# Performance work log

Measured on AMD Instinct MI355X. Metric: run time of the kernel, lower is better.

## Reference

```python
import jax, jax.numpy as jnp
import numpy as np
from jax import lax

PIXEL_MAX = 255.0  # PSNR reference intensity, matches I=255 in the torch source


def setup_inputs() -> dict:
    key = jax.random.key(0)
    k1, k2 = jax.random.split(key)
    # RGBA image and RGBA kernel, 0..255 pixel range (PSNR uses I=255)
    x = jax.random.uniform(k1, (1, 4, 2048, 2048), dtype=jnp.float32) * PIXEL_MAX
    kernel = jax.random.uniform(k2, (1, 4, 16, 16), dtype=jnp.float32) * PIXEL_MAX
    return {"x": x, "kernel": kernel}


def reference(x, kernel):
    """Fused equivalent of: unfold every (Hk,Wk) window, alpha-blend it with the
    kernel using the kernel's alpha channel, then per-window PSNR vs the kernel.

    alpha_blend(x_win, k, a) = (1-a)*x_win + a*k  with a = k_alpha/255, so
    blended - k = (1-a)*(x_win - k), hence per-window per-channel MSE is a
    weighted sliding-window sum: mean_ij w_ij*(x-k)^2 with w = (1-a)^2.
    Expanding (x-k)^2 lets us use three depthwise VALID correlations instead of
    materializing the [L,C,Hk,Wk] unfold+repeat tensor.
    """
    C, Hk, Wk = kernel.shape[1], kernel.shape[2], kernel.shape[3]
    k = kernel[0]                       # (C, Hk, Wk)
    alpha = k[3] / PIXEL_MAX            # (Hk, Wk), alpha plane (channel 3)
    w = (1.0 - alpha) ** 2              # per-tap weight, shared across channels

    dn = ("NCHW", "OIHW", "NCHW")
    w_dw = jnp.broadcast_to(w, (C, 1, Hk, Wk))   # depthwise weights
    kw_dw = (k * w)[:, None]                      # (C, 1, Hk, Wk)

    def corr(inp, wt):
        return lax.conv_general_dilated(
            inp, wt, window_strides=(1, 1), padding="VALID",
            dimension_numbers=dn, feature_group_count=C)

    Sxx = corr(x * x, w_dw)                        # (1, C, H', W') sum w*x^2
    Sxk = corr(x, kw_dw)                           # (1, C, H', W') sum w*x*k
    Skk = jnp.sum(k * k * w, axis=(-2, -1))[None, :, None, None]  # sum w*k^2

    mse = (Sxx - 2.0 * Sxk + Skk) / (Hk * Wk)      # (1, C, H', W')
    psnr = jnp.mean(20.0 * jnp.log10(PIXEL_MAX / jnp.sqrt(mse)), axis=1)  # mean over C
    return psnr[0]                                  # (H-Hk+1, W-Wk+1)
```

## Files before the change

kernel.cpp:

```cpp
#include <hip/hip_runtime.h>
#include <hip/hip_bf16.h>
#include <math.h>

#define XDIM 2048
#define OW   2033
#define TR   32
#define TC   256
#define XWP  272
#define PH   16

typedef __bf16 bf16x8 __attribute__((ext_vector_type(8)));
typedef float  f32x16 __attribute__((ext_vector_type(16)));

union U128 { uint4 u; bf16x8 v; };

__device__ __forceinline__ unsigned short bfbits(float f) {
    return __builtin_bit_cast(unsigned short, __float2bfloat16(f));
}
__device__ __forceinline__ unsigned int packx(float f) {
    return ((unsigned int)bfbits(f) << 16) | (unsigned int)bfbits(f * f);
}
__device__ __forceinline__ int slz(int c) {
    return c ^ (((c >> 2) & 7) << 1);
}

__global__ __launch_bounds__(256) void psnr_mfma_kernel(
    const float* __restrict__ x,
    const float* __restrict__ kern,
    float* __restrict__ out)
{
    __shared__ __align__(16) uint2 xtp[PH][XWP];
    __shared__ __align__(16) unsigned int wt[4][17 * 20];
    __shared__ float skkArr[4];

    const int tid  = threadIdx.x;
    const int lane = tid & 63;
    const int wv   = tid >> 6;
    const int nn   = lane & 31;
    const int hf   = lane >> 5;

    const int r0 = blockIdx.y * TR;
    const int c0 = blockIdx.x * TC;

    {
        float k0 = kern[tid], k1 = kern[256 + tid], k2 = kern[512 + tid], k3 = kern[768 + tid];
        float a  = k3 * (1.0f / 255.0f);
        float om = 1.0f - a;
        float w  = om * om;
        int i = tid >> 4, j = tid & 15;
        unsigned int wlo = (unsigned int)bfbits(w);
        wt[0][i * 20 + j] = ((unsigned int)bfbits(-2.0f * w * k0) << 16) | wlo;
        wt[1][i * 20 + j] = ((unsigned int)bfbits(-2.0f * w * k1) << 16) | wlo;
        wt[2][i * 20 + j] = ((unsigned int)bfbits(-2.0f * w * k2) << 16) | wlo;
        wt[3][i * 20 + j] = ((unsigned int)bfbits(-2.0f * w * k3) << 16) | wlo;
        if (tid < 80) {
            int c = tid / 20, wd = tid % 20;
            wt[c][16 * 20 + wd] = 0u;
        }
        float4* red = reinterpret_cast<float4*>(&xtp[0][0]);
        red[tid] = make_float4(w*k0*k0, w*k1*k1, w*k2*k2, w*k3*k3);
        __syncthreads();
        #pragma unroll
        for (int s = 128; s > 0; s >>= 1) {
            if (tid < s) {
                float4 o = red[tid + s], m = red[tid];
                m.x += o.x; m.y += o.y; m.z += o.z; m.w += o.w;
                red[tid] = m;
            }
            __syncthreads();
        }
        if (tid == 0) {
            float4 r0v = red[0];
            skkArr[0] = r0v.x; skkArr[1] = r0v.y; skkArr[2] = r0v.z; skkArr[3] = r0v.w;
        }
    }

    f32x16 psum0, psum1;
    #pragma unroll
    for (int q = 0; q < 16; ++q) { psum0[q] = 0.0f; psum1[q] = 0.0f; }

    const int xbase = nn + 4 * hf;
    const int wvoff = (wv << 6);
    const int p0 = slz(xbase)      + wvoff, p1 = slz(xbase + 2)  + wvoff;
    const int p2 = slz(xbase + 8)  + wvoff, p3 = slz(xbase + 10) + wvoff;
    const int p4 = slz(xbase + 32) + wvoff, p5 = slz(xbase + 34) + wvoff;
    const int p6 = slz(xbase + 40) + wvoff, p7 = slz(xbase + 42) + wvoff;

    for (int ch = 0; ch < 4; ++ch) {
        const float* __restrict__ xc = x + ((size_t)ch << 22);

        f32x16 acc0, acc1;
        #pragma unroll
        for (int q = 0; q < 16; ++q) { acc0[q] = 0.0f; acc1[q] = 0.0f; }

        #pragma unroll
        for (int ph = 0; ph < 3; ++ph) {
            const int base = ph * PH;
            const int nr   = (ph == 2) ? 15 : 16;

            __syncthreads();
            for (int idx = tid; idx < nr * 68; idx += 256) {
                int row = idx / 68;
                int it  = idx - row * 68;
                int gr  = r0 + base + row; if (gr > XDIM - 1) gr = XDIM - 1;
                int gc  = c0 + it * 4;
                const float* rp = xc + (size_t)gr * XDIM;
                float4 v;
                if (gc + 3 <= XDIM - 1) {
                    v = *reinterpret_cast<const float4*>(rp + gc);
                } else {
                    int e0 = gc     < XDIM ? gc     : XDIM - 1;
                    int e1 = gc + 1 < XDIM ? gc + 1 : XDIM - 1;
                    int e2 = gc + 2 < XDIM ? gc + 2 : XDIM - 1;
                    int e3 = gc + 3 < XDIM ? gc + 3 : XDIM - 1;
                    v = make_float4(rp[e0], rp[e1], rp[e2], rp[e3]);
                }
                int e4 = gc + 4 < XDIM ? gc + 4 : XDIM - 1;
                float x4 = rp[e4];

                unsigned int P0 = packx(v.x), P1 = packx(v.y), P2 = packx(v.z),
                             P3 = packx(v.w), P4 = packx(x4);
                int s   = (it & 7) << 1;
                int sl0 = (4 * it)     ^ s;
                int sl2 = (4 * it + 2) ^ s;
                uint2* bb = &xtp[row][0];
                *reinterpret_cast<uint4*>(bb + sl0) = make_uint4(P0, P1, P1, P2);
                *reinterpret_cast<uint4*>(bb + sl2) = make_uint4(P2, P3, P3, P4);
            }
            __syncthreads();

            const unsigned int* __restrict__ wch = &wt[ch][0];
            for (int r = 0; r < nr; ++r) {
                int ip = base + r;
                unsigned int d = (unsigned int)(ip - nn);
                unsigned int wrow = (d > 15u) ? 16u : d;
                U128 alo, ahi;
                alo.u = *reinterpret_cast<const uint4*>(wch + wrow * 20 + hf * 4);
                ahi.u = *reinterpret_cast<const uint4*>(wch + wrow * 20 + 8 + hf * 4);

                const uint2* __restrict__ bp = &xtp[r][0];
                U128 blo0, bhi0, blo1, bhi1;
                { uint2 a0 = bp[p0], a1 = bp[p1]; blo0.u = make_uint4(a0.x, a0.y, a1.x, a1.y); }
                { uint2 a0 = bp[p2], a1 = bp[p3]; bhi0.u = make_uint4(a0.x, a0.y, a1.x, a1.y); }
                { uint2 a0 = bp[p4], a1 = bp[p5]; blo1.u = make_uint4(a0.x, a0.y, a1.x, a1.y); }
                { uint2 a0 = bp[p6], a1 = bp[p7]; bhi1.u = make_uint4(a0.x, a0.y, a1.x, a1.y); }

                acc0 = __builtin_amdgcn_mfma_f32_32x32x16_bf16(alo.v, blo0.v, acc0, 0, 0, 0);
                acc0 = __builtin_amdgcn_mfma_f32_32x32x16_bf16(ahi.v, bhi0.v, acc0, 0, 0, 0);
                acc1 = __builtin_amdgcn_mfma_f32_32x32x16_bf16(alo.v, blo1.v, acc1, 0, 0, 0);
                acc1 = __builtin_amdgcn_mfma_f32_32x32x16_bf16(ahi.v, bhi1.v, acc1, 0, 0, 0);
            }
        }

        float sk = skkArr[ch];
        #pragma unroll
        for (int q = 0; q < 16; ++q) {
            float m0 = (acc0[q] + sk) * (1.0f / 256.0f);
            float m1 = (acc1[q] + sk) * (1.0f / 256.0f);
            psum0[q] += __log2f(m0);
            psum1[q] += __log2f(m1);
        }
    }

    const float BASE = 48.130803608679344f;
    const float SC   = 2.5f * 0.3010299956639812f;
    const int col0 = c0 + (wv << 6) + nn;
    const int col1 = col0 + 32;
    #pragma unroll
    for (int q = 0; q < 16; ++q) {
        int row = r0 + (q & 3) + ((q >> 2) << 3) + (hf << 2);
        if (row < OW) {
            float* orow = out + (size_t)row * OW;
            if (col0 < OW) orow[col0] = BASE - SC * psum0[q];
            if (col1 < OW) orow[col1] = BASE - SC * psum1[q];
        }
    }
}

extern "C" void kernel_launch(void* const* d_in, const int* in_sizes, int n_in,
                              void* d_out, int out_size, void* d_ws, size_t ws_size,
                              hipStream_t stream) {
    (void)in_sizes; (void)n_in; (void)d_ws; (void)ws_size; (void)out_size;
    const float* x    = (const float*)d_in[0];
    const float* kern = (const float*)d_in[1];
    float* out        = (float*)d_out;

    dim3 grid(XDIM / TC, (OW + TR - 1) / TR);
    psnr_mfma_kernel<<<grid, 256, 0, stream>>>(x, kern, out);
}
```

Measured before the change: 66.09 us.

## Double-buffer LDS tiles with register prefetch across flattened channel/phase loop

Flattens the channel and row-phase loops into one 12-step pipeline and double-buffers the packed bf16 tile in shared memory. Global loads for step p+2 are issued into registers while step p+1 is packed and written, which overlaps memory latency with MFMA work and halves the barriers per step. Packing now uses a single v_cvt_pk_bf16_f32 instruction. The cost is doubled LDS and more live registers, which may lower occupancy. The last phase now loads 16 rows instead of 15.

After: 68.08 us. +3.0%, slower.

```diff
diff --git a/kernel.cpp b/kernel.cpp
--- a/kernel.cpp
+++ b/kernel.cpp
@@ -8,6 +8,7 @@
 #define TC   256
 #define XWP  272
 #define PH   16
+#define NP   12
 
 typedef __bf16 bf16x8 __attribute__((ext_vector_type(8)));
 typedef float  f32x16 __attribute__((ext_vector_type(16)));
@@ -18,7 +19,9 @@
     return __builtin_bit_cast(unsigned short, __float2bfloat16(f));
 }
 __device__ __forceinline__ unsigned int packx(float f) {
-    return ((unsigned int)bfbits(f) << 16) | (unsigned int)bfbits(f * f);
+    unsigned int r;
+    asm("v_cvt_pk_bf16_f32 %0, %1, %2" : "=v"(r) : "v"(f * f), "v"(f));
+    return r;
 }
 __device__ __forceinline__ int slz(int c) {
     return c ^ (((c >> 2) & 7) << 1);
@@ -29,7 +32,7 @@
     const float* __restrict__ kern,
     float* __restrict__ out)
 {
-    __shared__ __align__(16) uint2 xtp[PH][XWP];
+    __shared__ __align__(16) uint2 xtp[2][PH][XWP];
     __shared__ __align__(16) unsigned int wt[4][17 * 20];
     __shared__ float skkArr[4];
 
@@ -41,6 +44,60 @@
 
     const int r0 = blockIdx.y * TR;
     const int c0 = blockIdx.x * TC;
+
+    float4 pf[5];
+    float  pe[5];
+
+    auto issue = [&](int p) {
+        int ch = p / 3, ph = p - 3 * ch;
+        const float* __restrict__ xc = x + ((size_t)ch << 22);
+        const int rbase = r0 + ph * PH;
+        #pragma unroll
+        for (int t = 0; t < 5; ++t) {
+            int idx = tid + 256 * t;
+            if (idx < PH * 68) {
+                int row = idx / 68;
+                int it  = idx - row * 68;
+                int gr  = rbase + row; if (gr > XDIM - 1) gr = XDIM - 1;
+                int gc  = c0 + it * 4;
+                const float* rp = xc + (size_t)gr * XDIM;
+                if (gc + 3 <= XDIM - 1) {
+                    pf[t] = *reinterpret_cast<const float4*>(rp + gc);
+                } else {
+                    int e0 = gc     < XDIM ? gc     : XDIM - 1;
+                    int e1 = gc + 1 < XDIM ? gc + 1 : XDIM - 1;
+                    int e2 = gc + 2 < XDIM ? gc + 2 : XDIM - 1;
+                    int e3 = gc + 3 < XDIM ? gc + 3 : XDIM - 1;
+                    pf[t] = make_float4(rp[e0], rp[e1], rp[e2], rp[e3]);
+                }
+                int e4 = gc + 4 < XDIM ? gc + 4 : XDIM - 1;
+                pe[t] = rp[e4];
+            }
+        }
+    };
+
+    auto wrt = [&](int p) {
+        uint2* __restrict__ buf = &xtp[p & 1][0][0];
+        #pragma unroll
+        for (int t = 0; t < 5; ++t) {
+            int idx = tid + 256 * t;
+            if (idx < PH * 68) {
+                int row = idx / 68;
+                int it  = idx - row * 68;
+                float4 v = pf[t];
+                unsigned int P0 = packx(v.x), P1 = packx(v.y), P2 = packx(v.z),
+                             P3 = packx(v.w), P4 = packx(pe[t]);
+                int s   = (it & 7) << 1;
+                int sl0 = (4 * it)     ^ s;
+                int sl2 = (4 * it + 2) ^ s;
+                uint2* bb = buf + row * XWP;
+                *reinterpret_cast<uint4*>(bb + sl0) = make_uint4(P0, P1, P1, P2);
+                *reinterpret_cast<uint4*>(bb + sl2) = make_uint4(P2, P3, P3, P4);
+            }
+        }
+    };
+
+    issue(0);
 
     {
         float k0 = kern[tid], k1 = kern[256 + tid], k2 = kern[512 + tid], k3 = kern[768 + tid];
@@ -57,7 +114,7 @@
             int c = tid / 20, wd = tid % 20;
             wt[c][16 * 20 + wd] = 0u;
         }
-        float4* red = reinterpret_cast<float4*>(&xtp[0][0]);
+        float4* red = reinterpret_cast<float4*>(&xtp[0][0][0]);
         red[tid] = make_float4(w*k0*k0, w*k1*k1, w*k2*k2, w*k3*k3);
         __syncthreads();
         #pragma unroll
@@ -73,9 +130,14 @@
             float4 r0v = red[0];
             skkArr[0] = r0v.x; skkArr[1] = r0v.y; skkArr[2] = r0v.z; skkArr[3] = r0v.w;
         }
+        __syncthreads();
     }
 
-    f32x16 psum0, psum1;
+    wrt(0);
+    issue(1);
+    __syncthreads();
+
+    f32x16 acc0, acc1, psum0, psum1;
     #pragma unroll
     for (int q = 0; q < 16; ++q) { psum0[q] = 0.0f; psum1[q] = 0.0f; }
 
@@ -86,79 +148,54 @@
     const int p4 = slz(xbase + 32) + wvoff, p5 = slz(xbase + 34) + wvoff;
     const int p6 = slz(xbase + 40) + wvoff, p7 = slz(xbase + 42) + wvoff;
 
-    for (int ch = 0; ch < 4; ++ch) {
-        const float* __restrict__ xc = x + ((size_t)ch << 22);
-
-        f32x16 acc0, acc1;
-        #pragma unroll
-        for (int q = 0; q < 16; ++q) { acc0[q] = 0.0f; acc1[q] = 0.0f; }
-
-        #pragma unroll
-        for (int ph = 0; ph < 3; ++ph) {
-            const int base = ph * PH;
-            const int nr   = (ph == 2) ? 15 : 16;
-
+    for (int p = 0; p < NP; ++p) {
+        const int ch  = p / 3;
+        const int ph  = p - 3 * ch;
+        const int nr  = (ph == 2) ? 15 : 16;
+
+        if (ph == 0) {
+            #pragma unroll
+            for (int q = 0; q < 16; ++q) { acc0[q] = 0.0f; acc1[q] = 0.0f; }
+        }
+
+        const unsigned int* __restrict__ wch = &wt[ch][0];
+        const uint2* __restrict__ bbase = &xtp[p & 1][0][0];
+        for (int r = 0; r < nr; ++r) {
+            int ip = ph * PH + r;
+            unsigned int d = (unsigned int)(ip - nn);
+            unsigned int wrow = (d > 15u) ? 16u : d;
+            U128 alo, ahi;
+            alo.u = *reinterpret_cast<const uint4*>(wch + wrow * 20 + hf * 4);
+            ahi.u = *reinterpret_cast<const uint4*>(wch + wrow * 20 + 8 + hf * 4);
+
+            const uint2* __restrict__ bp = bbase + r * XWP;
+            U128 blo0, bhi0, blo1, bhi1;
+            { uint2 a0 = bp[p0], a1 = bp[p1]; blo0.u = make_uint4(a0.x, a0.y, a1.x, a1.y); }
+            { uint2 a0 = bp[p2], a1 = bp[p3]; bhi0.u = make_uint4(a0.x, a0.y, a1.x, a1.y); }
+            { uint2 a0 = bp[p4], a1 = bp[p5]; blo1.u = make_uint4(a0.x, a0.y, a1.x, a1.y); }
+            { uint2 a0 = bp[p6], a1 = bp[p7]; bhi1.u = make_uint4(a0.x, a0.y, a1.x, a1.y); }
+
+            acc0 = __builtin_amdgcn_mfma_f32_32x32x16_bf16(alo.v, blo0.v, acc0, 0, 0, 0);
+            acc0 = __builtin_amdgcn_mfma_f32_32x32x16_bf16(ahi.v, bhi0.v, acc0, 0, 0, 0);
+            acc1 = __builtin_amdgcn_mfma_f32_32x32x16_bf16(alo.v, blo1.v, acc1, 0, 0, 0);
+            acc1 = __builtin_amdgcn_mfma_f32_32x32x16_bf16(ahi.v, bhi1.v, acc1, 0, 0, 0);
+        }
+
+        if (ph == 2) {
+            float sk = skkArr[ch];
+            #pragma unroll
+            for (int q = 0; q < 16; ++q) {
+                float m0 = (acc0[q] + sk) * (1.0f / 256.0f);
+                float m1 = (acc1[q] + sk) * (1.0f / 256.0f);
+                psum0[q] += __log2f(m0);
+                psum1[q] += __log2f(m1);
+            }
+        }
+
+        if (p + 1 < NP) {
+            wrt(p + 1);
+            if (p + 2 < NP) issue(p + 2);
             __syncthreads();
-            for (int idx = tid; idx < nr * 68; idx += 256) {
-                int row = idx / 68;
-                int it  = idx - row * 68;
-                int gr  = r0 + base + row; if (gr > XDIM - 1) gr = XDIM - 1;
-                int gc  = c0 + it * 4;
-                const float* rp = xc + (size_t)gr * XDIM;
-                float4 v;
-                if (gc + 3 <= XDIM - 1) {
-                    v = *reinterpret_cast<const float4*>(rp + gc);
-                } else {
-                    int e0 = gc     < XDIM ? gc     : XDIM - 1;
-                    int e1 = gc + 1 < XDIM ? gc + 1 : XDIM - 1;
-                    int e2 = gc + 2 < XDIM ? gc + 2 : XDIM - 1;
-                    int e3 = gc + 3 < XDIM ? gc + 3 : XDIM - 1;
-                    v = make_float4(rp[e0], rp[e1], rp[e2], rp[e3]);
-                }
-                int e4 = gc + 4 < XDIM ? gc + 4 : XDIM - 1;
-                float x4 = rp[e4];
-
-                unsigned int P0 = packx(v.x), P1 = packx(v.y), P2 = packx(v.z),
-                             P3 = packx(v.w), P4 = packx(x4);
-                int s   = (it & 7) << 1;
-                int sl0 = (4 * it)     ^ s;
-                int sl2 = (4 * it + 2) ^ s;
-                uint2* bb = &xtp[row][0];
-                *reinterpret_cast<uint4*>(bb + sl0) = make_uint4(P0, P1, P1, P2);
-                *reinterpret_cast<uint4*>(bb + sl2) = make_uint4(P2, P3, P3, P4);
-            }
-            __syncthreads();
-
-            const unsigned int* __restrict__ wch = &wt[ch][0];
-            for (int r = 0; r < nr; ++r) {
-                int ip = base + r;
-                unsigned int d = (unsigned int)(ip - nn);
-                unsigned int wrow = (d > 15u) ? 16u : d;
-                U128 alo, ahi;
-                alo.u = *reinterpret_cast<const uint4*>(wch + wrow * 20 + hf * 4);
-                ahi.u = *reinterpret_cast<const uint4*>(wch + wrow * 20 + 8 + hf * 4);
-
-                const uint2* __restrict__ bp = &xtp[r][0];
-                U128 blo0, bhi0, blo1, bhi1;
-                { uint2 a0 = bp[p0], a1 = bp[p1]; blo0.u = make_uint4(a0.x, a0.y, a1.x, a1.y); }
-                { uint2 a0 = bp[p2], a1 = bp[p3]; bhi0.u = make_uint4(a0.x, a0.y, a1.x, a1.y); }
-                { uint2 a0 = bp[p4], a1 = bp[p5]; blo1.u = make_uint4(a0.x, a0.y, a1.x, a1.y); }
-                { uint2 a0 = bp[p6], a1 = bp[p7]; bhi1.u = make_uint4(a0.x, a0.y, a1.x, a1.y); }
-
-                acc0 = __builtin_amdgcn_mfma_f32_32x32x16_bf16(alo.v, blo0.v, acc0, 0, 0, 0);
-                acc0 = __builtin_amdgcn_mfma_f32_32x32x16_bf16(ahi.v, bhi0.v, acc0, 0, 0, 0);
-                acc1 = __builtin_amdgcn_mfma_f32_32x32x16_bf16(alo.v, blo1.v, acc1, 0, 0, 0);
-                acc1 = __builtin_amdgcn_mfma_f32_32x32x16_bf16(ahi.v, bhi1.v, acc1, 0, 0, 0);
-            }
-        }
-
-        float sk = skkArr[ch];
-        #pragma unroll
-        for (int q = 0; q < 16; ++q) {
-            float m0 = (acc0[q] + sk) * (1.0f / 256.0f);
-            float m1 = (acc1[q] + sk) * (1.0f / 256.0f);
-            psum0[q] += __log2f(m0);
-            psum1[q] += __log2f(m1);
         }
     }
 
```

## Per-wave double-buffered register-prefetch pipeline replacing block-wide LDS staging

Applied to the files above, without the earlier changes.

Replaces the block-wide shared tile and its two __syncthreads per phase with a per-wave double-buffered LDS buffer. Each wave loads only its own 80-column slab, in 8-row phases flattened across channels. Global loads for phase p+2 are issued into registers while phase p computes, so memory latency overlaps MFMA work without block barriers. It also uses a packed v_cvt_pk_bf16_f32 instruction for the x/x^2 conversion. The cost is more redundant halo loads per wave (80 vs 64 columns), extra registers for the prefetch, and reliance on wave-local LDS coherence without barriers.

Measured after the change: 74.01 us. 1.12x slower.

```diff
diff --git a/kernel.cpp b/kernel.cpp
--- a/kernel.cpp
+++ b/kernel.cpp
@@ -6,8 +6,9 @@
 #define OW   2033
 #define TR   32
 #define TC   256
-#define XWP  272
-#define PH   16
+#define WPC  80
+#define PH   8
+#define NPH  24
 
 typedef __bf16 bf16x8 __attribute__((ext_vector_type(8)));
 typedef float  f32x16 __attribute__((ext_vector_type(16)));
@@ -18,18 +19,18 @@
     return __builtin_bit_cast(unsigned short, __float2bfloat16(f));
 }
 __device__ __forceinline__ unsigned int packx(float f) {
-    return ((unsigned int)bfbits(f) << 16) | (unsigned int)bfbits(f * f);
-}
-__device__ __forceinline__ int slz(int c) {
-    return c ^ (((c >> 2) & 7) << 1);
-}
+    unsigned int r;
+    asm("v_cvt_pk_bf16_f32 %0, %1, %2" : "=v"(r) : "v"(f * f), "v"(f));
+    return r;
+}
+__device__ __forceinline__ int slz(int c) { return c ^ (((c >> 2) & 7) << 1); }
 
 __global__ __launch_bounds__(256) void psnr_mfma_kernel(
     const float* __restrict__ x,
     const float* __restrict__ kern,
     float* __restrict__ out)
 {
-    __shared__ __align__(16) uint2 xtp[PH][XWP];
+    __shared__ __align__(16) uint2 wbuf[4][2][PH][WPC];
     __shared__ __align__(16) unsigned int wt[4][17 * 20];
     __shared__ float skkArr[4];
 
@@ -39,8 +40,61 @@
     const int nn   = lane & 31;
     const int hf   = lane >> 5;
 
-    const int r0 = blockIdx.y * TR;
-    const int c0 = blockIdx.x * TC;
+    const int r0  = blockIdx.y * TR;
+    const int c0  = blockIdx.x * TC;
+    const int c0w = c0 + (wv << 6);
+
+    float4 pf0, pf1, pf2;
+    float  pe0, pe1, pe2;
+
+    auto ld1 = [&](int q, int ch, int it, float4& v4, float& v1) {
+        unsigned int row = (unsigned int)it / 20u;
+        int cc = (it - (int)row * 20) * 4;
+        int gr = r0 + q * PH + (int)row; if (gr > XDIM - 1) gr = XDIM - 1;
+        int gc = c0w + cc;
+        const float* rp = x + ((size_t)ch << 22) + (size_t)gr * XDIM;
+        if (gc + 3 <= XDIM - 1) {
+            v4 = *reinterpret_cast<const float4*>(rp + gc);
+        } else {
+            int e0 = gc     < XDIM ? gc     : XDIM - 1;
+            int e1 = gc + 1 < XDIM ? gc + 1 : XDIM - 1;
+            int e2 = gc + 2 < XDIM ? gc + 2 : XDIM - 1;
+            int e3 = gc + 3 < XDIM ? gc + 3 : XDIM - 1;
+            v4 = make_float4(rp[e0], rp[e1], rp[e2], rp[e3]);
+        }
+        int e4 = gc + 4 < XDIM ? gc + 4 : XDIM - 1;
+        v1 = rp[e4];
+    };
+
+    auto issue = [&](int p) {
+        int ch = (int)(((unsigned)p * 2731u) >> 14);
+        int q  = p - 6 * ch;
+        ld1(q, ch, lane,       pf0, pe0);
+        ld1(q, ch, lane + 64,  pf1, pe1);
+        if (lane < 32) ld1(q, ch, lane + 128, pf2, pe2);
+    };
+
+    auto w1 = [&](uint2* buf, int it, const float4& v4, float v1) {
+        unsigned int row = (unsigned int)it / 20u;
+        int iw = it - (int)row * 20;
+        unsigned int P0 = packx(v4.x), P1 = packx(v4.y), P2 = packx(v4.z),
+                     P3 = packx(v4.w), P4 = packx(v1);
+        int s   = (iw & 7) << 1;
+        int sl0 = (4 * iw)     ^ s;
+        int sl2 = (4 * iw + 2) ^ s;
+        uint2* bb = buf + row * WPC;
+        *reinterpret_cast<uint4*>(bb + sl0) = make_uint4(P0, P1, P1, P2);
+        *reinterpret_cast<uint4*>(bb + sl2) = make_uint4(P2, P3, P3, P4);
+    };
+
+    auto wrt = [&](int p) {
+        uint2* buf = &wbuf[wv][p & 1][0][0];
+        w1(buf, lane,      pf0, pe0);
+        w1(buf, lane + 64, pf1, pe1);
+        if (lane < 32) w1(buf, lane + 128, pf2, pe2);
+    };
+
+    issue(0);
 
     {
         float k0 = kern[tid], k1 = kern[256 + tid], k2 = kern[512 + tid], k3 = kern[768 + tid];
@@ -57,7 +111,7 @@
             int c = tid / 20, wd = tid % 20;
             wt[c][16 * 20 + wd] = 0u;
         }
-        float4* red = reinterpret_cast<float4*>(&xtp[0][0]);
+        float4* red = reinterpret_cast<float4*>(&wbuf[0][0][0][0]);
         red[tid] = make_float4(w*k0*k0, w*k1*k1, w*k2*k2, w*k3*k3);
         __syncthreads();
         #pragma unroll
@@ -73,77 +127,50 @@
             float4 r0v = red[0];
             skkArr[0] = r0v.x; skkArr[1] = r0v.y; skkArr[2] = r0v.z; skkArr[3] = r0v.w;
         }
+        __syncthreads();
     }
 
-    f32x16 psum0, psum1;
+    wrt(0);
+    issue(1);
+
+    f32x16 acc0, acc1, psum0, psum1;
     #pragma unroll
     for (int q = 0; q < 16; ++q) { psum0[q] = 0.0f; psum1[q] = 0.0f; }
 
-    const int xbase = nn + 4 * hf;
-    const int wvoff = (wv << 6);
-    const int p0 = slz(xbase)      + wvoff, p1 = slz(xbase + 2)  + wvoff;
-    const int p2 = slz(xbase + 8)  + wvoff, p3 = slz(xbase + 10) + wvoff;
-    const int p4 = slz(xbase + 32) + wvoff, p5 = slz(xbase + 34) + wvoff;
-    const int p6 = slz(xbase + 40) + wvoff, p7 = slz(xbase + 42) + wvoff;
-
-    for (int ch = 0; ch < 4; ++ch) {
-        const float* __restrict__ xc = x + ((size_t)ch << 22);
-
-        f32x16 acc0, acc1;
+    const int xb = nn + 4 * hf;
+    const int b0 = slz(xb),      b1 = slz(xb + 2);
+    const int b2 = slz(xb + 8),  b3 = slz(xb + 10);
+    const int b4 = slz(xb + 32), b5 = slz(xb + 34);
+    const int b6 = slz(xb + 40), b7 = slz(xb + 42);
+
+    for (int p = 0; p < NPH; ++p) {
+        int ch = (int)(((unsigned)p * 2731u) >> 14);
+        int q  = p - 6 * ch;
+
+        if (q == 0) {
+            #pragma unroll
+            for (int t = 0; t < 16; ++t) { acc0[t] = 0.0f; acc1[t] = 0.0f; }
+        }
+
+        const unsigned int* __restrict__ wch = &wt[ch][0];
+        const uint2* __restrict__ bbase = &wbuf[wv][p & 1][0][0];
+
         #pragma unroll
-        for (int q = 0; q < 16; ++q) { acc0[q] = 0.0f; acc1[q] = 0.0f; }
-
-        #pragma unroll
-        for (int ph = 0; ph < 3; ++ph) {
-            const int base = ph * PH;
-            const int nr   = (ph == 2) ? 15 : 16;
-
-            __syncthreads();
-            for (int idx = tid; idx < nr * 68; idx += 256) {
-                int row = idx / 68;
-                int it  = idx - row * 68;
-                int gr  = r0 + base + row; if (gr > XDIM - 1) gr = XDIM - 1;
-                int gc  = c0 + it * 4;
-                const float* rp = xc + (size_t)gr * XDIM;
-                float4 v;
-                if (gc + 3 <= XDIM - 1) {
-                    v = *reinterpret_cast<const float4*>(rp + gc);
-                } else {
-                    int e0 = gc     < XDIM ? gc     : XDIM - 1;
-                    int e1 = gc + 1 < XDIM ? gc + 1 : XDIM - 1;
-                    int e2 = gc + 2 < XDIM ? gc + 2 : XDIM - 1;
-                    int e3 = gc + 3 < XDIM ? gc + 3 : XDIM - 1;
-                    v = make_float4(rp[e0], rp[e1], rp[e2], rp[e3]);
-                }
-                int e4 = gc + 4 < XDIM ? gc + 4 : XDIM - 1;
-                float x4 = rp[e4];
-
-                unsigned int P0 = packx(v.x), P1 = packx(v.y), P2 = packx(v.z),
-                             P3 = packx(v.w), P4 = packx(x4);
-                int s   = (it & 7) << 1;
-                int sl0 = (4 * it)     ^ s;
-                int sl2 = (4 * it + 2) ^ s;
-                uint2* bb = &xtp[row][0];
-                *reinterpret_cast<uint4*>(bb + sl0) = make_uint4(P0, P1, P1, P2);
-                *reinterpret_cast<uint4*>(bb + sl2) = make_uint4(P2, P3, P3, P4);
-            }
-            __syncthreads();
-
-            const unsigned int* __restrict__ wch = &wt[ch][0];
-            for (int r = 0; r < nr; ++r) {
-                int ip = base + r;
+        for (int r = 0; r < PH; ++r) {
+            int ip = q * PH + r;
+            if (ip < 47) {
                 unsigned int d = (unsigned int)(ip - nn);
                 unsigned int wrow = (d > 15u) ? 16u : d;
                 U128 alo, ahi;
                 alo.u = *reinterpret_cast<const uint4*>(wch + wrow * 20 + hf * 4);
                 ahi.u = *reinterpret_cast<const uint4*>(wch + wrow * 20 + 8 + hf * 4);
 
-                const uint2* __restrict__ bp = &xtp[r][0];
+                const uint2* __restrict__ bp = bbase + r * WPC;
                 U128 blo0, bhi0, blo1, bhi1;
-                { uint2 a0 = bp[p0], a1 = bp[p1]; blo0.u = make_uint4(a0.x, a0.y, a1.x, a1.y); }
-                { uint2 a0 = bp[p2], a1 = bp[p3]; bhi0.u = make_uint4(a0.x, a0.y, a1.x, a1.y); }
-                { uint2 a0 = bp[p4], a1 = bp[p5]; blo1.u = make_uint4(a0.x, a0.y, a1.x, a1.y); }
-                { uint2 a0 = bp[p6], a1 = bp[p7]; bhi1.u = make_uint4(a0.x, a0.y, a1.x, a1.y); }
+                { uint2 a0 = bp[b0], a1 = bp[b1]; blo0.u = make_uint4(a0.x, a0.y, a1.x, a1.y); }
+                { uint2 a0 = bp[b2], a1 = bp[b3]; bhi0.u = make_uint4(a0.x, a0.y, a1.x, a1.y); }
+                { uint2 a0 = bp[b4], a1 = bp[b5]; blo1.u = make_uint4(a0.x, a0.y, a1.x, a1.y); }
+                { uint2 a0 = bp[b6], a1 = bp[b7]; bhi1.u = make_uint4(a0.x, a0.y, a1.x, a1.y); }
 
                 acc0 = __builtin_amdgcn_mfma_f32_32x32x16_bf16(alo.v, blo0.v, acc0, 0, 0, 0);
                 acc0 = __builtin_amdgcn_mfma_f32_32x32x16_bf16(ahi.v, bhi0.v, acc0, 0, 0, 0);
@@ -152,27 +179,32 @@
             }
         }
 
-        float sk = skkArr[ch];
-        #pragma unroll
-        for (int q = 0; q < 16; ++q) {
-            float m0 = (acc0[q] + sk) * (1.0f / 256.0f);
-            float m1 = (acc1[q] + sk) * (1.0f / 256.0f);
-            psum0[q] += __log2f(m0);
-            psum1[q] += __log2f(m1);
-        }
+        if (q == 5) {
+            float sk = skkArr[ch];
+            #pragma unroll
+            for (int t = 0; t < 16; ++t) {
+                float m0 = (acc0[t] + sk) * (1.0f / 256.0f);
+                float m1 = (acc1[t] + sk) * (1.0f / 256.0f);
+                psum0[t] += __log2f(m0);
+                psum1[t] += __log2f(m1);
+            }
+        }
+
+        if (p + 1 < NPH) wrt(p + 1);
+        if (p + 2 < NPH) issue(p + 2);
     }
 
     const float BASE = 48.130803608679344f;
     const float SC   = 2.5f * 0.3010299956639812f;
-    const int col0 = c0 + (wv << 6) + nn;
+    const int col0 = c0w + nn;
     const int col1 = col0 + 32;
     #pragma unroll
-    for (int q = 0; q < 16; ++q) {
-        int row = r0 + (q & 3) + ((q >> 2) << 3) + (hf << 2);
+    for (int t = 0; t < 16; ++t) {
+        int row = r0 + (t & 3) + ((t >> 2) << 3) + (hf << 2);
         if (row < OW) {
             float* orow = out + (size_t)row * OW;
-            if (col0 < OW) orow[col0] = BASE - SC * psum0[q];
-            if (col1 < OW) orow[col1] = BASE - SC * psum1[q];
+            if (col0 < OW) orow[col0] = BASE - SC * psum0[t];
+            if (col1 < OW) orow[col1] = BASE - SC * psum1[t];
         }
     }
 }
```
